# Kernel optimization log

Hardware: AMD Instinct MI355X
Metric: run time of the kernel (lower is better)

Reference implementation:

```python
import jax, jax.numpy as jnp
import numpy as np

MUL = 128                      # multiplicity per irrep
DIMS = (1, 3, 5)               # 2l+1 for l = 0, 1, 2
OFFS = (0, MUL, MUL * 4)       # start offsets of each l-block
TOT = MUL * 9                  # 1152 = total irrep dim
NM = 3 * MUL                   # num_mul = 384


def _split(x):
    # x: [B, 1152] -> list of [B, 128, 2l+1]
    return [x[:, OFFS[i]:OFFS[i] + MUL * DIMS[i]].reshape(-1, MUL, DIMS[i]) for i in range(3)]


def _merge(parts):
    return jnp.concatenate([p.reshape(p.shape[0], -1) for p in parts], axis=-1)


def irrep_linear(x, W, b0):
    # e3nn o3.Linear: per-l mixing of multiplicities, / sqrt(fan_in), bias on scalars only
    parts = _split(x)
    out = [jnp.einsum('nui,uv->nvi', parts[i], W[i]) / np.sqrt(MUL) for i in range(3)]
    out = [out[0] + b0[None, :, None], out[1], out[2]]
    return _merge(out)


def norm_gate_fn(x, W1, b1, W2, b2):
    # QHNet NormGate: [scalars | per-channel norms] -> MLP -> gate non-scalar channels
    parts = _split(x)
    x0 = parts[0][:, :, 0]
    n1 = jnp.sqrt(jnp.sum(parts[1] ** 2, axis=-1))
    n2 = jnp.sqrt(jnp.sum(parts[2] ** 2, axis=-1))
    f0 = jnp.concatenate([x0, n1, n2], axis=-1)          # [B, 384]
    g = jax.nn.silu(f0 @ W1 + b1) @ W2 + b2              # [B, 384]
    g0, g1, g2 = g[:, :MUL], g[:, MUL:2 * MUL], g[:, 2 * MUL:]
    return _merge([g0[:, :, None], parts[1] * g1[:, :, None], parts[2] * g2[:, :, None]])


def ssp(x):
    # shifted softplus
    return jax.nn.softplus(x) - np.log(2.0)


def setup_inputs() -> dict:
    key = jax.random.key(0)
    ks = jax.random.split(key, 24)
    N, E, EA, H = 4096, 65536, 64, 8
    f32 = jnp.float32
    inp = {}
    inp['node_attr'] = jax.random.normal(ks[0], (N, TOT), f32)
    inp['edge_attr'] = jax.random.uniform(ks[1], (E, EA), f32)
    inp['dst'] = jax.random.randint(ks[2], (E,), 0, N)
    inp['src'] = jax.random.randint(ks[3], (E,), 0, N)
    inp['node_pair_attr'] = jax.random.normal(ks[4], (E, TOT), f32)
    # irrep linears (linear_node_pair_inner, linear_node_pair_n, linear_node_pair)
    inp['W_inner'] = jax.random.normal(ks[5], (3, MUL, MUL), f32)
    inp['b_inner'] = jnp.zeros((MUL,), f32)
    inp['W_n'] = jax.random.normal(ks[6], (3, MUL, MUL), f32)
    inp['b_n'] = jnp.zeros((MUL,), f32)
    inp['W_out'] = jax.random.normal(ks[7], (3, MUL, MUL), f32)
    inp['b_out'] = jnp.zeros((MUL,), f32)
    # norm_gate_pre MLP
    inp['ng_pre_W1'] = jax.random.normal(ks[8], (NM, NM), f32) / np.sqrt(NM)
    inp['ng_pre_b1'] = jnp.zeros((NM,), f32)
    inp['ng_pre_W2'] = jax.random.normal(ks[9], (NM, NM), f32) / np.sqrt(NM)
    inp['ng_pre_b2'] = jnp.zeros((NM,), f32)
    # norm_gate MLP
    inp['ng_W1'] = jax.random.normal(ks[10], (NM, NM), f32) / np.sqrt(NM)
    inp['ng_b1'] = jnp.zeros((NM,), f32)
    inp['ng_W2'] = jax.random.normal(ks[11], (NM, NM), f32) / np.sqrt(NM)
    inp['ng_b2'] = jnp.zeros((NM,), f32)
    # fc_node_pair: e3nn FullyConnectedNet [64, 8, 128], no biases, /sqrt(fan_in) in fwd
    inp['fcE_W1'] = jax.random.normal(ks[12], (EA, H), f32)
    inp['fcE_W2'] = jax.random.normal(ks[13], (H, MUL), f32)
    # self.fc: Linear(384,128) + SiLU + Linear(128,128)
    inp['fc_W1'] = jax.random.normal(ks[14], (NM, MUL), f32) / np.sqrt(NM)
    inp['fc_b1'] = jnp.zeros((MUL,), f32)
    inp['fc_W2'] = jax.random.normal(ks[15], (MUL, MUL), f32) / np.sqrt(MUL)
    inp['fc_b2'] = jnp.zeros((MUL,), f32)
    return inp


def reference(node_attr, edge_attr, dst, src, node_pair_attr,
              W_inner, b_inner, W_n, b_n, W_out, b_out,
              ng_pre_W1, ng_pre_b1, ng_pre_W2, ng_pre_b2,
              ng_W1, ng_b1, ng_W2, ng_b2,
              fcE_W1, fcE_W2, fc_W1, fc_b1, fc_W2, fc_b2):
    # s0: scalar invariants from inner products of gathered pair features
    na0 = irrep_linear(node_attr, W_inner, b_inner)
    p_d, p_s = _split(na0[dst]), _split(na0[src])
    ip1 = jnp.sum(p_d[1] * p_s[1], axis=-1) / np.sqrt(3.0)   # [E, 128]
    ip2 = jnp.sum(p_d[2] * p_s[2], axis=-1) / np.sqrt(5.0)   # [E, 128]
    s0 = jnp.concatenate([0.5 * (p_d[0][:, :, 0] + p_s[0][:, :, 0]), ip1, ip2], axis=-1)  # [E, 384]

    na = norm_gate_fn(node_attr, ng_pre_W1, ng_pre_b1, ng_pre_W2, ng_pre_b2)
    na = irrep_linear(na, W_n, b_n)

    # edge gate: e3nn FCN (ssp, /sqrt(fan_in), no bias) * torch MLP(SiLU)
    we = ssp(edge_attr @ fcE_W1 / np.sqrt(edge_attr.shape[-1])) @ fcE_W2 / np.sqrt(fcE_W1.shape[-1])
    ws = jax.nn.silu(s0 @ fc_W1 + fc_b1) @ fc_W2 + fc_b2
    w = we * ws                                              # [E, 128]
    E = w.shape[0]
    total_orb = TOT // MUL                                   # 9
    w_full = jnp.broadcast_to(w[:, :, None], (E, MUL, total_orb)).reshape(E, TOT)

    node_pair = (na[src] + na[dst]) * w_full
    node_pair = norm_gate_fn(node_pair, ng_W1, ng_b1, ng_W2, ng_b2)
    node_pair = irrep_linear(node_pair, W_out, b_out)
    return node_pair + node_pair_attr                        # resnet
```

## Files before the change

### kernel.cpp

```cpp
#include <hip/hip_runtime.h>
#include <cmath>


typedef unsigned short u16;
typedef __bf16 v8bf __attribute__((ext_vector_type(8)));
typedef float  v4f  __attribute__((ext_vector_type(4)));

#define NN 4096
#define EE 65536

__device__ __forceinline__ float b2f(u16 u) {
    union { float f; unsigned i; } x; x.i = ((unsigned)u) << 16; return x.f;
}
__device__ __forceinline__ u16 f2b(float f) {
    union { float f; unsigned i; } x; x.f = f;
    unsigned i = x.i;
    return (u16)((i + 0x7FFFu + ((i >> 16) & 1u)) >> 16);
}

struct GemmP {
    const u16* A; int lda;
    const u16* Bt;
    int M, K, N;
    float alpha;
    const float* bias;
    u16* outB;
    const u16* mult;
    const float* add;
    float* outF;
};

template <int EPI>
__global__ __launch_bounds__(256)
void gemm_k(GemmP p) {
    __shared__ __attribute__((aligned(16))) u16 Al[64][40];
    __shared__ __attribute__((aligned(16))) u16 Bl[64][40];

    const int m0 = blockIdx.x * 64;
    const int n0 = blockIdx.y * 64;
    const int t  = threadIdx.x;
    const int lane = t & 63;
    const int wid  = t >> 6;
    const int wm = (wid & 1) * 32;
    const int wn = (wid >> 1) * 32;
    const int sm = t >> 2;
    const int sk = (t & 3) * 8;
    const int fr = lane & 15;
    const int q  = lane >> 4;

    v4f acc[2][2] = {};

    const u16* Ag = p.A  + (size_t)(m0 + sm) * p.lda + sk;
    const u16* Bg = p.Bt + (size_t)(n0 + sm) * p.K   + sk;

    for (int k0 = 0; k0 < p.K; k0 += 32) {
        uint4 av = *(const uint4*)(Ag + k0);
        uint4 bv = *(const uint4*)(Bg + k0);
        __syncthreads();
        *(uint4*)(&Al[sm][sk]) = av;
        *(uint4*)(&Bl[sm][sk]) = bv;
        __syncthreads();
        v8bf a0 = *(const v8bf*)(&Al[wm +      fr][q * 8]);
        v8bf a1 = *(const v8bf*)(&Al[wm + 16 + fr][q * 8]);
        v8bf b0 = *(const v8bf*)(&Bl[wn +      fr][q * 8]);
        v8bf b1 = *(const v8bf*)(&Bl[wn + 16 + fr][q * 8]);
        acc[0][0] = __builtin_amdgcn_mfma_f32_16x16x32_bf16(a0, b0, acc[0][0], 0, 0, 0);
        acc[0][1] = __builtin_amdgcn_mfma_f32_16x16x32_bf16(a0, b1, acc[0][1], 0, 0, 0);
        acc[1][0] = __builtin_amdgcn_mfma_f32_16x16x32_bf16(a1, b0, acc[1][0], 0, 0, 0);
        acc[1][1] = __builtin_amdgcn_mfma_f32_16x16x32_bf16(a1, b1, acc[1][1], 0, 0, 0);
    }

#pragma unroll
    for (int i = 0; i < 2; i++) {
#pragma unroll
        for (int j = 0; j < 2; j++) {
            const int colg = n0 + wn + j * 16 + fr;
            const float bc = p.bias ? p.bias[colg] : 0.0f;
#pragma unroll
            for (int r = 0; r < 4; r++) {
                const int rowg = m0 + wm + i * 16 + q * 4 + r;
                float v = acc[i][j][r] * p.alpha + bc;
                if constexpr (EPI == 0) {
                    p.outB[(size_t)rowg * p.N + colg] = f2b(v);
                } else if constexpr (EPI == 1) {
                    v = v / (1.0f + __expf(-v));
                    p.outB[(size_t)rowg * p.N + colg] = f2b(v);
                } else if constexpr (EPI == 2) {
                    v *= b2f(p.mult[(size_t)rowg * p.N + colg]);
                    p.outB[(size_t)rowg * p.N + colg] = f2b(v);
                } else {
                    constexpr int DIM = (EPI == 3) ? 1 : ((EPI == 4) ? 3 : 5);
                    constexpr int OFF = (EPI == 3) ? 0 : ((EPI == 4) ? 128 : 512);
                    const int e  = rowg / DIM;
                    const int ii = rowg - e * DIM;
                    const size_t idx = (size_t)e * 1152 + OFF + colg * DIM + ii;
                    p.outF[idx] = v + p.add[idx];
                }
            }
        }
    }
}

struct CvtP { const float* src[15]; u16* dst[15]; int K[15]; int N[15]; };

__global__ void cvt_k(CvtP p) {
    const int j = blockIdx.y;
    const float* s = p.src[j];
    u16* d = p.dst[j];
    const int K = p.K[j], N = p.N[j], tot = K * N;
    for (int idx = blockIdx.x * blockDim.x + threadIdx.x; idx < tot;
         idx += gridDim.x * blockDim.x) {
        const int n = idx / K, k = idx - n * K;
        d[idx] = f2b(s[(size_t)k * N + n]);
    }
}

__global__ void node_prep_k(const float* __restrict__ na, u16* __restrict__ x1p,
                            u16* __restrict__ x2p, u16* __restrict__ f0n) {
    const int idx = blockIdx.x * blockDim.x + threadIdx.x;
    if (idx >= NN * 128) return;
    const int n = idx >> 7, u = idx & 127;
    const float* row = na + (size_t)n * 1152;
    f0n[(size_t)n * 384 + u] = f2b(row[u]);
    float s1 = 0.f;
#pragma unroll
    for (int i = 0; i < 3; i++) {
        float v = row[128 + u * 3 + i];
        x1p[((size_t)(n * 3 + i)) * 128 + u] = f2b(v);
        s1 += v * v;
    }
    f0n[(size_t)n * 384 + 128 + u] = f2b(sqrtf(s1));
    float s2 = 0.f;
#pragma unroll
    for (int i = 0; i < 5; i++) {
        float v = row[512 + u * 5 + i];
        x2p[((size_t)(n * 5 + i)) * 128 + u] = f2b(v);
        s2 += v * v;
    }
    f0n[(size_t)n * 384 + 256 + u] = f2b(sqrtf(s2));
}

__global__ void node_gate_k(const float* __restrict__ na, const u16* __restrict__ gn,
                            u16* __restrict__ h1p, u16* __restrict__ h2p) {
    const int idx = blockIdx.x * blockDim.x + threadIdx.x;
    if (idx >= NN * 128) return;
    const int n = idx >> 7, u = idx & 127;
    const float* row = na + (size_t)n * 1152;
    const float g1 = b2f(gn[(size_t)n * 384 + 128 + u]);
#pragma unroll
    for (int i = 0; i < 3; i++)
        h1p[((size_t)(n * 3 + i)) * 128 + u] = f2b(row[128 + u * 3 + i] * g1);
    const float g2 = b2f(gn[(size_t)n * 384 + 256 + u]);
#pragma unroll
    for (int i = 0; i < 5; i++)
        h2p[((size_t)(n * 5 + i)) * 128 + u] = f2b(row[512 + u * 5 + i] * g2);
}

__global__ void we_k(const float* __restrict__ ea, const float* __restrict__ W1,
                     const float* __restrict__ W2, u16* __restrict__ we) {
    const int lane = threadIdx.x & 63;
    const int e = blockIdx.x * 4 + (threadIdx.x >> 6);
    const float a = ea[(size_t)e * 64 + lane];
    float t8[8];
#pragma unroll
    for (int h = 0; h < 8; h++) {
        float s = a * W1[lane * 8 + h];
#pragma unroll
        for (int m = 1; m < 64; m <<= 1) s += __shfl_xor(s, m, 64);
        const float x = s * 0.125f;
        const float sp = (x > 20.f) ? x : log1pf(__expf(x));
        t8[h] = sp - 0.6931471805599453f;
    }
    float v0 = 0.f, v1 = 0.f;
#pragma unroll
    for (int h = 0; h < 8; h++) {
        v0 += t8[h] * W2[h * 128 + lane];
        v1 += t8[h] * W2[h * 128 + 64 + lane];
    }
    we[(size_t)e * 128 + lane]      = f2b(v0 * 0.3535533905932738f);
    we[(size_t)e * 128 + 64 + lane] = f2b(v1 * 0.3535533905932738f);
}

__global__ void s0_k(const int* __restrict__ dst, const int* __restrict__ src,
                     const u16* __restrict__ na0_0, const u16* __restrict__ na0_1p,
                     const u16* __restrict__ na0_2p, u16* __restrict__ s0) {
    const int e = blockIdx.x, u = threadIdx.x;
    const int d = dst[e], s = src[e];
    const float v0 = 0.5f * (b2f(na0_0[(size_t)d * 128 + u]) + b2f(na0_0[(size_t)s * 128 + u]));
    float ip1 = 0.f;
#pragma unroll
    for (int i = 0; i < 3; i++)
        ip1 += b2f(na0_1p[((size_t)(d * 3 + i)) * 128 + u]) *
               b2f(na0_1p[((size_t)(s * 3 + i)) * 128 + u]);
    float ip2 = 0.f;
#pragma unroll
    for (int i = 0; i < 5; i++)
        ip2 += b2f(na0_2p[((size_t)(d * 5 + i)) * 128 + u]) *
               b2f(na0_2p[((size_t)(s * 5 + i)) * 128 + u]);
    s0[(size_t)e * 384 + u]       = f2b(v0);
    s0[(size_t)e * 384 + 128 + u] = f2b(ip1 * 0.57735026918962576f);
    s0[(size_t)e * 384 + 256 + u] = f2b(ip2 * 0.44721359549995794f);
}

__global__ void pair_k(const int* __restrict__ dst, const int* __restrict__ src,
                       const u16* __restrict__ na_0, const u16* __restrict__ na_1p,
                       const u16* __restrict__ na_2p, const u16* __restrict__ w,
                       u16* __restrict__ f0e, u16* __restrict__ np1p,
                       u16* __restrict__ np2p) {
    __shared__ float wr[128];
    const int e = blockIdx.x, u = threadIdx.x;
    wr[u] = b2f(w[(size_t)e * 128 + u]);
    __syncthreads();
    const int d = dst[e], s = src[e];
    const float v0 = (b2f(na_0[(size_t)d * 128 + u]) + b2f(na_0[(size_t)s * 128 + u])) * wr[u / 9];
    f0e[(size_t)e * 384 + u] = f2b(v0);
    float n1 = 0.f;
#pragma unroll
    for (int i = 0; i < 3; i++) {
        const int t = 128 + u * 3 + i;
        const float v = (b2f(na_1p[((size_t)(d * 3 + i)) * 128 + u]) +
                         b2f(na_1p[((size_t)(s * 3 + i)) * 128 + u])) * wr[t / 9];
        np1p[((size_t)(e * 3 + i)) * 128 + u] = f2b(v);
        n1 += v * v;
    }
    f0e[(size_t)e * 384 + 128 + u] = f2b(sqrtf(n1));
    float n2 = 0.f;
#pragma unroll
    for (int i = 0; i < 5; i++) {
        const int t = 512 + u * 5 + i;
        const float v = (b2f(na_2p[((size_t)(d * 5 + i)) * 128 + u]) +
                         b2f(na_2p[((size_t)(s * 5 + i)) * 128 + u])) * wr[t / 9];
        np2p[((size_t)(e * 5 + i)) * 128 + u] = f2b(v);
        n2 += v * v;
    }
    f0e[(size_t)e * 384 + 256 + u] = f2b(sqrtf(n2));
}

__global__ void gate_k(const u16* __restrict__ ge, u16* __restrict__ np1p,
                       u16* __restrict__ np2p) {
    const int idx = blockIdx.x * blockDim.x + threadIdx.x;
    if (idx >= EE * 128) return;
    const int e = idx >> 7, u = idx & 127;
    const float g1 = b2f(ge[(size_t)e * 384 + 128 + u]);
#pragma unroll
    for (int i = 0; i < 3; i++) {
        const size_t pth = ((size_t)(e * 3 + i)) * 128 + u;
        np1p[pth] = f2b(b2f(np1p[pth]) * g1);
    }
    const float g2 = b2f(ge[(size_t)e * 384 + 256 + u]);
#pragma unroll
    for (int i = 0; i < 5; i++) {
        const size_t pth = ((size_t)(e * 5 + i)) * 128 + u;
        np2p[pth] = f2b(b2f(np2p[pth]) * g2);
    }
}

static inline void launch_gemm(hipStream_t st, int epi, const u16* A, int lda,
                               const u16* Bt, int M, int K, int N, float alpha,
                               const float* bias, u16* outB, const u16* mult,
                               const float* add, float* outF) {
    GemmP p{A, lda, Bt, M, K, N, alpha, bias, outB, mult, add, outF};
    dim3 g(M / 64, N / 64), b(256);
    switch (epi) {
        case 0: gemm_k<0><<<g, b, 0, st>>>(p); break;
        case 1: gemm_k<1><<<g, b, 0, st>>>(p); break;
        case 2: gemm_k<2><<<g, b, 0, st>>>(p); break;
        case 3: gemm_k<3><<<g, b, 0, st>>>(p); break;
        case 4: gemm_k<4><<<g, b, 0, st>>>(p); break;
        case 5: gemm_k<5><<<g, b, 0, st>>>(p); break;
    }
}

extern "C" void kernel_launch(void* const* d_in, const int* in_sizes, int n_in,
                              void* d_out, int out_size, void* d_ws, size_t ws_size,
                              hipStream_t stream) {
    (void)in_sizes; (void)n_in; (void)out_size; (void)ws_size;
    const float* node_attr = (const float*)d_in[0];
    const float* edge_attr = (const float*)d_in[1];
    const int*   dst       = (const int*)d_in[2];
    const int*   src       = (const int*)d_in[3];
    const float* npa       = (const float*)d_in[4];
    const float* W_inner   = (const float*)d_in[5];
    const float* b_inner   = (const float*)d_in[6];
    const float* W_n       = (const float*)d_in[7];
    const float* b_n       = (const float*)d_in[8];
    const float* W_out     = (const float*)d_in[9];
    const float* b_out     = (const float*)d_in[10];
    const float* pre_W1    = (const float*)d_in[11];
    const float* pre_b1    = (const float*)d_in[12];
    const float* pre_W2    = (const float*)d_in[13];
    const float* pre_b2    = (const float*)d_in[14];
    const float* ng_W1     = (const float*)d_in[15];
    const float* ng_b1     = (const float*)d_in[16];
    const float* ng_W2     = (const float*)d_in[17];
    const float* ng_b2     = (const float*)d_in[18];
    const float* fcE_W1    = (const float*)d_in[19];
    const float* fcE_W2    = (const float*)d_in[20];
    const float* fc_W1     = (const float*)d_in[21];
    const float* fc_b1     = (const float*)d_in[22];
    const float* fc_W2     = (const float*)d_in[23];
    const float* fc_b2     = (const float*)d_in[24];
    float* out = (float*)d_out;
    u16* W = (u16*)d_ws;

    u16* wbT_inner = W;
    u16* wbT_n     = W + 49152;
    u16* wbT_out   = W + 98304;
    u16* wbT_pre1  = W + 147456;
    u16* wbT_pre2  = W + 294912;
    u16* wbT_ng1   = W + 442368;
    u16* wbT_ng2   = W + 589824;
    u16* wbT_fc1   = W + 737280;
    u16* wbT_fc2   = W + 786432;
    u16* R1   = W + 802816;
    u16* x1p  = R1;
    u16* x2p  = R1 + 1572864;
    u16* f0n  = R1 + 4194304;
    u16* t1n  = R1 + 5767168;
    u16* gn   = R1 + 7340032;
    u16* hn1p = R1 + 8912896;
    u16* hn2p = R1 + 10485760;
    u16* s0   = R1;
    u16* t1e  = R1;
    u16* na0_0  = W + 25968640;
    u16* na0_1p = na0_0 + 524288;
    u16* na0_2p = na0_1p + 1572864;
    u16* na_0   = na0_2p + 2621440;
    u16* na_1p  = na_0 + 524288;
    u16* na_2p  = na_1p + 1572864;
    u16* ws1    = na_2p + 2621440;
    u16* weB    = ws1 + 8388608;
    u16* wB     = weB + 8388608;
    u16* f0e    = wB + 8388608;
    u16* ge     = f0e;
    u16* np1p   = f0e + 25165824;
    u16* np2p   = np1p + 25165824;

    const float ISQ = 0.08838834764831845f;

    CvtP cp;
    const float* srcs[15] = {W_inner, W_inner + 16384, W_inner + 32768,
                             W_n, W_n + 16384, W_n + 32768,
                             W_out, W_out + 16384, W_out + 32768,
                             pre_W1, pre_W2, ng_W1, ng_W2, fc_W1, fc_W2};
    u16* dsts[15] = {wbT_inner, wbT_inner + 16384, wbT_inner + 32768,
                     wbT_n, wbT_n + 16384, wbT_n + 32768,
                     wbT_out, wbT_out + 16384, wbT_out + 32768,
                     wbT_pre1, wbT_pre2, wbT_ng1, wbT_ng2, wbT_fc1, wbT_fc2};
    const int Ks[15] = {128,128,128,128,128,128,128,128,128,384,384,384,384,384,128};
    const int Ns[15] = {128,128,128,128,128,128,128,128,128,384,384,384,384,128,128};
    for (int j = 0; j < 15; j++) { cp.src[j]=srcs[j]; cp.dst[j]=dsts[j]; cp.K[j]=Ks[j]; cp.N[j]=Ns[j]; }
    cvt_k<<<dim3(64, 15), dim3(256), 0, stream>>>(cp);

    node_prep_k<<<dim3(2048), dim3(256), 0, stream>>>(node_attr, x1p, x2p, f0n);

    launch_gemm(stream, 0, f0n, 384, wbT_inner,          4096, 128, 128, ISQ, b_inner, na0_0, 0, 0, 0);
    launch_gemm(stream, 0, x1p, 128, wbT_inner + 16384, 12288, 128, 128, ISQ, nullptr, na0_1p, 0, 0, 0);
    launch_gemm(stream, 0, x2p, 128, wbT_inner + 32768, 20480, 128, 128, ISQ, nullptr, na0_2p, 0, 0, 0);

    launch_gemm(stream, 1, f0n, 384, wbT_pre1, 4096, 384, 384, 1.f, pre_b1, t1n, 0, 0, 0);
    launch_gemm(stream, 0, t1n, 384, wbT_pre2, 4096, 384, 384, 1.f, pre_b2, gn, 0, 0, 0);
    node_gate_k<<<dim3(2048), dim3(256), 0, stream>>>(node_attr, gn, hn1p, hn2p);

    launch_gemm(stream, 0, gn,   384, wbT_n,          4096, 128, 128, ISQ, b_n,     na_0,  0, 0, 0);
    launch_gemm(stream, 0, hn1p, 128, wbT_n + 16384, 12288, 128, 128, ISQ, nullptr, na_1p, 0, 0, 0);
    launch_gemm(stream, 0, hn2p, 128, wbT_n + 32768, 20480, 128, 128, ISQ, nullptr, na_2p, 0, 0, 0);

    we_k<<<dim3(EE / 4), dim3(256), 0, stream>>>(edge_attr, fcE_W1, fcE_W2, weB);

    s0_k<<<dim3(EE), dim3(128), 0, stream>>>(dst, src, na0_0, na0_1p, na0_2p, s0);

    launch_gemm(stream, 1, s0,  384, wbT_fc1, EE, 384, 128, 1.f, fc_b1, ws1, 0,   0, 0);
    launch_gemm(stream, 2, ws1, 128, wbT_fc2, EE, 128, 128, 1.f, fc_b2, wB,  weB, 0, 0);

    pair_k<<<dim3(EE), dim3(128), 0, stream>>>(dst, src, na_0, na_1p, na_2p, wB, f0e, np1p, np2p);

    launch_gemm(stream, 1, f0e, 384, wbT_ng1, EE, 384, 384, 1.f, ng_b1, t1e, 0, 0, 0);
    launch_gemm(stream, 0, t1e, 384, wbT_ng2, EE, 384, 384, 1.f, ng_b2, ge,  0, 0, 0);
    gate_k<<<dim3(32768), dim3(256), 0, stream>>>(ge, np1p, np2p);

    launch_gemm(stream, 3, ge,   384, wbT_out,          EE,     128, 128, ISQ, b_out,   0, 0, npa, out);
    launch_gemm(stream, 4, np1p, 128, wbT_out + 16384,  EE * 3, 128, 128, ISQ, nullptr, 0, 0, npa, out);
    launch_gemm(stream, 5, np2p, 128, wbT_out + 32768,  EE * 5, 128, 128, ISQ, nullptr, 0, 0, npa, out);
}
```

Baseline: 1.225 ms.

## Fuse edge pair gather, norm-gate MLP, gating and output linear into one kernel

Result: no change. 1.221 ms (-0.3%).

```diff
diff --git a/kernel.cpp b/kernel.cpp
--- a/kernel.cpp
+++ b/kernel.cpp
@@ -8,6 +8,8 @@
 
 #define NN 4096
 #define EE 65536
+
+#define MFMA16 __builtin_amdgcn_mfma_f32_16x16x32_bf16
 
 __device__ __forceinline__ float b2f(u16 u) {
     union { float f; unsigned i; } x; x.i = ((unsigned)u) << 16; return x.f;
@@ -26,8 +28,6 @@
     const float* bias;
     u16* outB;
     const u16* mult;
-    const float* add;
-    float* outF;
 };
 
 template <int EPI>
@@ -64,10 +64,10 @@
         v8bf a1 = *(const v8bf*)(&Al[wm + 16 + fr][q * 8]);
         v8bf b0 = *(const v8bf*)(&Bl[wn +      fr][q * 8]);
         v8bf b1 = *(const v8bf*)(&Bl[wn + 16 + fr][q * 8]);
-        acc[0][0] = __builtin_amdgcn_mfma_f32_16x16x32_bf16(a0, b0, acc[0][0], 0, 0, 0);
-        acc[0][1] = __builtin_amdgcn_mfma_f32_16x16x32_bf16(a0, b1, acc[0][1], 0, 0, 0);
-        acc[1][0] = __builtin_amdgcn_mfma_f32_16x16x32_bf16(a1, b0, acc[1][0], 0, 0, 0);
-        acc[1][1] = __builtin_amdgcn_mfma_f32_16x16x32_bf16(a1, b1, acc[1][1], 0, 0, 0);
+        acc[0][0] = MFMA16(a0, b0, acc[0][0], 0, 0, 0);
+        acc[0][1] = MFMA16(a0, b1, acc[0][1], 0, 0, 0);
+        acc[1][0] = MFMA16(a1, b0, acc[1][0], 0, 0, 0);
+        acc[1][1] = MFMA16(a1, b1, acc[1][1], 0, 0, 0);
     }
 
 #pragma unroll
@@ -85,16 +85,9 @@
                 } else if constexpr (EPI == 1) {
                     v = v / (1.0f + __expf(-v));
                     p.outB[(size_t)rowg * p.N + colg] = f2b(v);
-                } else if constexpr (EPI == 2) {
+                } else {
                     v *= b2f(p.mult[(size_t)rowg * p.N + colg]);
                     p.outB[(size_t)rowg * p.N + colg] = f2b(v);
-                } else {
-                    constexpr int DIM = (EPI == 3) ? 1 : ((EPI == 4) ? 3 : 5);
-                    constexpr int OFF = (EPI == 3) ? 0 : ((EPI == 4) ? 128 : 512);
-                    const int e  = rowg / DIM;
-                    const int ii = rowg - e * DIM;
-                    const size_t idx = (size_t)e * 1152 + OFF + colg * DIM + ii;
-                    p.outF[idx] = v + p.add[idx];
                 }
             }
         }
@@ -202,72 +195,256 @@
     s0[(size_t)e * 384 + 256 + u] = f2b(ip2 * 0.44721359549995794f);
 }
 
-__global__ void pair_k(const int* __restrict__ dst, const int* __restrict__ src,
-                       const u16* __restrict__ na_0, const u16* __restrict__ na_1p,
-                       const u16* __restrict__ na_2p, const u16* __restrict__ w,
-                       u16* __restrict__ f0e, u16* __restrict__ np1p,
-                       u16* __restrict__ np2p) {
-    __shared__ float wr[128];
-    const int e = blockIdx.x, u = threadIdx.x;
-    wr[u] = b2f(w[(size_t)e * 128 + u]);
+__global__ __launch_bounds__(256, 2)
+void edge_fused_k(const int* __restrict__ dst, const int* __restrict__ src,
+                  const u16* __restrict__ na_0, const u16* __restrict__ na_1p,
+                  const u16* __restrict__ na_2p, const u16* __restrict__ wB,
+                  const u16* __restrict__ W1t, const float* __restrict__ b1,
+                  const u16* __restrict__ W2t, const float* __restrict__ b2,
+                  const u16* __restrict__ Wot, const float* __restrict__ bo,
+                  const float* __restrict__ npa, float* __restrict__ out) {
+    __shared__ __attribute__((aligned(16))) u16 bufA[32][392];
+    __shared__ __attribute__((aligned(16))) u16 bufN[21760];
+    __shared__ int dstS[32], srcS[32];
+    __shared__ u16 wS[32][128];
+
+    u16 (*T1)[392]   = (u16 (*)[392])bufN;
+    u16 (*NP)[136]   = (u16 (*)[136])bufN;
+    float (*STG)[68] = (float (*)[68])bufN;
+
+    const int e0 = blockIdx.x * 32;
+    const int t = threadIdx.x;
+    const int lane = t & 63, wid = t >> 6;
+    const int fr = lane & 15, q = lane >> 4;
+    const float ISQ = 0.08838834764831845f;
+
+    if (t < 32) { dstS[t] = dst[e0 + t]; srcS[t] = src[e0 + t]; }
+#pragma unroll
+    for (int rep = 0; rep < 16; rep++) {
+        const int idx = rep * 256 + t;
+        ((u16*)wS)[idx] = wB[(size_t)e0 * 128 + idx];
+    }
     __syncthreads();
-    const int d = dst[e], s = src[e];
-    const float v0 = (b2f(na_0[(size_t)d * 128 + u]) + b2f(na_0[(size_t)s * 128 + u])) * wr[u / 9];
-    f0e[(size_t)e * 384 + u] = f2b(v0);
-    float n1 = 0.f;
-#pragma unroll
-    for (int i = 0; i < 3; i++) {
-        const int t = 128 + u * 3 + i;
+
+    for (int rep = 0; rep < 16; rep++) {
+        const int idx = rep * 256 + t;
+        const int e = idx >> 7, u = idx & 127;
+        const int d = dstS[e], s = srcS[e];
+        const float v0 = (b2f(na_0[(size_t)d * 128 + u]) + b2f(na_0[(size_t)s * 128 + u]))
+                         * b2f(wS[e][u / 9]);
+        bufA[e][u] = f2b(v0);
+        float n1 = 0.f;
+#pragma unroll
+        for (int i = 0; i < 3; i++) {
+            const float v = (b2f(na_1p[((size_t)(d * 3 + i)) * 128 + u]) +
+                             b2f(na_1p[((size_t)(s * 3 + i)) * 128 + u]))
+                            * b2f(wS[e][(128 + u * 3 + i) / 9]);
+            n1 += v * v;
+        }
+        bufA[e][128 + u] = f2b(sqrtf(n1));
+        float n2 = 0.f;
+#pragma unroll
+        for (int i = 0; i < 5; i++) {
+            const float v = (b2f(na_2p[((size_t)(d * 5 + i)) * 128 + u]) +
+                             b2f(na_2p[((size_t)(s * 5 + i)) * 128 + u]))
+                            * b2f(wS[e][(512 + u * 5 + i) / 9]);
+            n2 += v * v;
+        }
+        bufA[e][256 + u] = f2b(sqrtf(n2));
+    }
+    __syncthreads();
+
+    {
+        const int wn = wid * 96;
+        v4f acc[2][6] = {};
+        for (int k0 = 0; k0 < 384; k0 += 32) {
+            const v8bf a0 = *(const v8bf*)&bufA[fr][k0 + q * 8];
+            const v8bf a1 = *(const v8bf*)&bufA[16 + fr][k0 + q * 8];
+#pragma unroll
+            for (int j = 0; j < 6; j++) {
+                const v8bf b = *(const v8bf*)(W1t + (size_t)(wn + j * 16 + fr) * 384 + k0 + q * 8);
+                acc[0][j] = MFMA16(a0, b, acc[0][j], 0, 0, 0);
+                acc[1][j] = MFMA16(a1, b, acc[1][j], 0, 0, 0);
+            }
+        }
+#pragma unroll
+        for (int i = 0; i < 2; i++)
+#pragma unroll
+            for (int j = 0; j < 6; j++) {
+                const int col = wn + j * 16 + fr;
+                const float bb = b1[col];
+#pragma unroll
+                for (int r = 0; r < 4; r++) {
+                    const float v = acc[i][j][r] + bb;
+                    T1[i * 16 + q * 4 + r][col] = f2b(v / (1.f + __expf(-v)));
+                }
+            }
+    }
+    __syncthreads();
+
+    {
+        const int wn = wid * 96;
+        v4f acc[2][6] = {};
+        for (int k0 = 0; k0 < 384; k0 += 32) {
+            const v8bf a0 = *(const v8bf*)&T1[fr][k0 + q * 8];
+            const v8bf a1 = *(const v8bf*)&T1[16 + fr][k0 + q * 8];
+#pragma unroll
+            for (int j = 0; j < 6; j++) {
+                const v8bf b = *(const v8bf*)(W2t + (size_t)(wn + j * 16 + fr) * 384 + k0 + q * 8);
+                acc[0][j] = MFMA16(a0, b, acc[0][j], 0, 0, 0);
+                acc[1][j] = MFMA16(a1, b, acc[1][j], 0, 0, 0);
+            }
+        }
+#pragma unroll
+        for (int i = 0; i < 2; i++)
+#pragma unroll
+            for (int j = 0; j < 6; j++) {
+                const int col = wn + j * 16 + fr;
+                const float bb = b2[col];
+#pragma unroll
+                for (int r = 0; r < 4; r++)
+                    bufA[i * 16 + q * 4 + r][col] = f2b(acc[i][j][r] + bb);
+            }
+    }
+    __syncthreads();
+
+    {
+        const int wn = wid * 32;
+        v4f acc[2][2] = {};
+        for (int k0 = 0; k0 < 128; k0 += 32) {
+            const v8bf a0 = *(const v8bf*)&bufA[fr][k0 + q * 8];
+            const v8bf a1 = *(const v8bf*)&bufA[16 + fr][k0 + q * 8];
+#pragma unroll
+            for (int j = 0; j < 2; j++) {
+                const v8bf b = *(const v8bf*)(Wot + (size_t)(wn + j * 16 + fr) * 128 + k0 + q * 8);
+                acc[0][j] = MFMA16(a0, b, acc[0][j], 0, 0, 0);
+                acc[1][j] = MFMA16(a1, b, acc[1][j], 0, 0, 0);
+            }
+        }
+#pragma unroll
+        for (int i = 0; i < 2; i++)
+#pragma unroll
+            for (int j = 0; j < 2; j++) {
+                const int col = wn + j * 16 + fr;
+                const float bb = bo[col];
+#pragma unroll
+                for (int r = 0; r < 4; r++) {
+                    const size_t o = (size_t)(e0 + i * 16 + q * 4 + r) * 1152 + col;
+                    out[o] = acc[i][j][r] * ISQ + bb + npa[o];
+                }
+            }
+    }
+
+    for (int rep = 0; rep < 48; rep++) {
+        const int idx = rep * 256 + t;
+        const int row = idx >> 7, u = idx & 127;
+        const int e = row / 3, i = row - e * 3;
+        const int d = dstS[e], s = srcS[e];
         const float v = (b2f(na_1p[((size_t)(d * 3 + i)) * 128 + u]) +
-                         b2f(na_1p[((size_t)(s * 3 + i)) * 128 + u])) * wr[t / 9];
-        np1p[((size_t)(e * 3 + i)) * 128 + u] = f2b(v);
-        n1 += v * v;
-    }
-    f0e[(size_t)e * 384 + 128 + u] = f2b(sqrtf(n1));
-    float n2 = 0.f;
-#pragma unroll
-    for (int i = 0; i < 5; i++) {
-        const int t = 512 + u * 5 + i;
+                         b2f(na_1p[((size_t)(s * 3 + i)) * 128 + u]))
+                        * b2f(wS[e][(128 + u * 3 + i) / 9]);
+        NP[row][u] = f2b(v * b2f(bufA[e][128 + u]));
+    }
+    __syncthreads();
+    {
+        const int wm = (wid & 1) * 48, wn = (wid >> 1) * 64;
+        const u16* Wo1 = Wot + 16384;
+        v4f acc[3][4] = {};
+        for (int k0 = 0; k0 < 128; k0 += 32) {
+            v8bf a[3];
+#pragma unroll
+            for (int mi = 0; mi < 3; mi++)
+                a[mi] = *(const v8bf*)&NP[wm + mi * 16 + fr][k0 + q * 8];
+#pragma unroll
+            for (int j = 0; j < 4; j++) {
+                const v8bf b = *(const v8bf*)(Wo1 + (size_t)(wn + j * 16 + fr) * 128 + k0 + q * 8);
+#pragma unroll
+                for (int mi = 0; mi < 3; mi++) acc[mi][j] = MFMA16(a[mi], b, acc[mi][j], 0, 0, 0);
+            }
+        }
+        __syncthreads();
+        for (int h = 0; h < 2; h++) {
+            if ((wid >> 1) == h) {
+#pragma unroll
+                for (int mi = 0; mi < 3; mi++)
+#pragma unroll
+                    for (int j = 0; j < 4; j++)
+#pragma unroll
+                        for (int r = 0; r < 4; r++)
+                            STG[wm + mi * 16 + q * 4 + r][j * 16 + fr] = acc[mi][j][r] * ISQ;
+            }
+            __syncthreads();
+            for (int rep = 0; rep < 24; rep++) {
+                const int idx = rep * 256 + t;
+                const int e = idx / 192, p = idx - e * 192;
+                const int c = p / 3, i = p - c * 3;
+                const size_t o = (size_t)(e0 + e) * 1152 + 128 + h * 192 + p;
+                out[o] = STG[e * 3 + i][c] + npa[o];
+            }
+            __syncthreads();
+        }
+    }
+
+    for (int rep = 0; rep < 80; rep++) {
+        const int idx = rep * 256 + t;
+        const int row = idx >> 7, u = idx & 127;
+        const int e = row / 5, i = row - e * 5;
+        const int d = dstS[e], s = srcS[e];
         const float v = (b2f(na_2p[((size_t)(d * 5 + i)) * 128 + u]) +
-                         b2f(na_2p[((size_t)(s * 5 + i)) * 128 + u])) * wr[t / 9];
-        np2p[((size_t)(e * 5 + i)) * 128 + u] = f2b(v);
-        n2 += v * v;
-    }
-    f0e[(size_t)e * 384 + 256 + u] = f2b(sqrtf(n2));
-}
-
-__global__ void gate_k(const u16* __restrict__ ge, u16* __restrict__ np1p,
-                       u16* __restrict__ np2p) {
-    const int idx = blockIdx.x * blockDim.x + threadIdx.x;
-    if (idx >= EE * 128) return;
-    const int e = idx >> 7, u = idx & 127;
-    const float g1 = b2f(ge[(size_t)e * 384 + 128 + u]);
-#pragma unroll
-    for (int i = 0; i < 3; i++) {
-        const size_t pth = ((size_t)(e * 3 + i)) * 128 + u;
-        np1p[pth] = f2b(b2f(np1p[pth]) * g1);
-    }
-    const float g2 = b2f(ge[(size_t)e * 384 + 256 + u]);
-#pragma unroll
-    for (int i = 0; i < 5; i++) {
-        const size_t pth = ((size_t)(e * 5 + i)) * 128 + u;
-        np2p[pth] = f2b(b2f(np2p[pth]) * g2);
+                         b2f(na_2p[((size_t)(s * 5 + i)) * 128 + u]))
+                        * b2f(wS[e][(512 + u * 5 + i) / 9]);
+        NP[row][u] = f2b(v * b2f(bufA[e][256 + u]));
+    }
+    __syncthreads();
+    {
+        const int wm = (wid & 1) * 80, wn = (wid >> 1) * 64;
+        const u16* Wo2 = Wot + 32768;
+        v4f acc[5][4] = {};
+        for (int k0 = 0; k0 < 128; k0 += 32) {
+            v8bf a[5];
+#pragma unroll
+            for (int mi = 0; mi < 5; mi++)
+                a[mi] = *(const v8bf*)&NP[wm + mi * 16 + fr][k0 + q * 8];
+#pragma unroll
+            for (int j = 0; j < 4; j++) {
+                const v8bf b = *(const v8bf*)(Wo2 + (size_t)(wn + j * 16 + fr) * 128 + k0 + q * 8);
+#pragma unroll
+                for (int mi = 0; mi < 5; mi++) acc[mi][j] = MFMA16(a[mi], b, acc[mi][j], 0, 0, 0);
+            }
+        }
+        __syncthreads();
+        for (int h = 0; h < 2; h++) {
+            if ((wid >> 1) == h) {
+#pragma unroll
+                for (int mi = 0; mi < 5; mi++)
+#pragma unroll
+                    for (int j = 0; j < 4; j++)
+#pragma unroll
+                        for (int r = 0; r < 4; r++)
+                            STG[wm + mi * 16 + q * 4 + r][j * 16 + fr] = acc[mi][j][r] * ISQ;
+            }
+            __syncthreads();
+            for (int rep = 0; rep < 40; rep++) {
+                const int idx = rep * 256 + t;
+                const int e = idx / 320, p = idx - e * 320;
+                const int c = p / 5, i = p - c * 5;
+                const size_t o = (size_t)(e0 + e) * 1152 + 512 + h * 320 + p;
+                out[o] = STG[e * 5 + i][c] + npa[o];
+            }
+            __syncthreads();
+        }
     }
 }
 
 static inline void launch_gemm(hipStream_t st, int epi, const u16* A, int lda,
                                const u16* Bt, int M, int K, int N, float alpha,
-                               const float* bias, u16* outB, const u16* mult,
-                               const float* add, float* outF) {
-    GemmP p{A, lda, Bt, M, K, N, alpha, bias, outB, mult, add, outF};
+                               const float* bias, u16* outB, const u16* mult) {
+    GemmP p{A, lda, Bt, M, K, N, alpha, bias, outB, mult};
     dim3 g(M / 64, N / 64), b(256);
     switch (epi) {
         case 0: gemm_k<0><<<g, b, 0, st>>>(p); break;
         case 1: gemm_k<1><<<g, b, 0, st>>>(p); break;
         case 2: gemm_k<2><<<g, b, 0, st>>>(p); break;
-        case 3: gemm_k<3><<<g, b, 0, st>>>(p); break;
-        case 4: gemm_k<4><<<g, b, 0, st>>>(p); break;
-        case 5: gemm_k<5><<<g, b, 0, st>>>(p); break;
     }
 }
 
@@ -321,7 +498,6 @@
     u16* hn1p = R1 + 8912896;
     u16* hn2p = R1 + 10485760;
     u16* s0   = R1;
-    u16* t1e  = R1;
     u16* na0_0  = W + 25968640;
     u16* na0_1p = na0_0 + 524288;
     u16* na0_2p = na0_1p + 1572864;
@@ -331,10 +507,6 @@
     u16* ws1    = na_2p + 2621440;
     u16* weB    = ws1 + 8388608;
     u16* wB     = weB + 8388608;
-    u16* f0e    = wB + 8388608;
-    u16* ge     = f0e;
-    u16* np1p   = f0e + 25165824;
-    u16* np2p   = np1p + 25165824;
 
     const float ISQ = 0.08838834764831845f;
 
@@ -354,32 +526,26 @@
 
     node_prep_k<<<dim3(2048), dim3(256), 0, stream>>>(node_attr, x1p, x2p, f0n);
 
-    launch_gemm(stream, 0, f0n, 384, wbT_inner,          4096, 128, 128, ISQ, b_inner, na0_0, 0, 0, 0);
-    launch_gemm(stream, 0, x1p, 128, wbT_inner + 16384, 12288, 128, 128, ISQ, nullptr, na0_1p, 0, 0, 0);
-    launch_gemm(stream, 0, x2p, 128, wbT_inner + 32768, 20480, 128, 128, ISQ, nullptr, na0_2p, 0, 0, 0);
-
-    launch_gemm(stream, 1, f0n, 384, wbT_pre1, 4096, 384, 384, 1.f, pre_b1, t1n, 0, 0, 0);
-    launch_gemm(stream, 0, t1n, 384, wbT_pre2, 4096, 384, 384, 1.f, pre_b2, gn, 0, 0, 0);
+    launch_gemm(stream, 0, f0n, 384, wbT_inner,          4096, 128, 128, ISQ, b_inner, na0_0, 0);
+    launch_gemm(stream, 0, x1p, 128, wbT_inner + 16384, 12288, 128, 128, ISQ, nullptr, na0_1p, 0);
+    launch_gemm(stream, 0, x2p, 128, wbT_inner + 32768, 20480, 128, 128, ISQ, nullptr, na0_2p, 0);
+
+    launch_gemm(stream, 1, f0n, 384, wbT_pre1, 4096, 384, 384, 1.f, pre_b1, t1n, 0);
+    launch_gemm(stream, 0, t1n, 384, wbT_pre2, 4096, 384, 384, 1.f, pre_b2, gn, 0);
     node_gate_k<<<dim3(2048), dim3(256), 0, stream>>>(node_attr, gn, hn1p, hn2p);
 
-    launch_gemm(stream, 0, gn,   384, wbT_n,          4096, 128, 128, ISQ, b_n,     na_0,  0, 0, 0);
-    launch_gemm(stream, 0, hn1p, 128, wbT_n + 16384, 12288, 128, 128, ISQ, nullptr, na_1p, 0, 0, 0);
-    launch_gemm(stream, 0, hn2p, 128, wbT_n + 32768, 20480, 128, 128, ISQ, nullptr, na_2p, 0, 0, 0);
+    launch_gemm(stream, 0, gn,   384, wbT_n,          4096, 128, 128, ISQ, b_n,     na_0,  0);
+    launch_gemm(stream, 0, hn1p, 128, wbT_n + 16384, 12288, 128, 128, ISQ, nullptr, na_1p, 0);
+    launch_gemm(stream, 0, hn2p, 128, wbT_n + 32768, 20480, 128, 128, ISQ, nullptr, na_2p, 0);
 
     we_k<<<dim3(EE / 4), dim3(256), 0, stream>>>(edge_attr, fcE_W1, fcE_W2, weB);
 
     s0_k<<<dim3(EE), dim3(128), 0, stream>>>(dst, src, na0_0, na0_1p, na0_2p, s0);
 
-    launch_gemm(stream, 1, s0,  384, wbT_fc1, EE, 384, 128, 1.f, fc_b1, ws1, 0,   0, 0);
-    launch_gemm(stream, 2, ws1, 128, wbT_fc2, EE, 128, 128, 1.f, fc_b2, wB,  weB, 0, 0);
-
-    pair_k<<<dim3(EE), dim3(128), 0, stream>>>(dst, src, na_0, na_1p, na_2p, wB, f0e, np1p, np2p);
-
-    launch_gemm(stream, 1, f0e, 384, wbT_ng1, EE, 384, 384, 1.f, ng_b1, t1e, 0, 0, 0);
-    launch_gemm(stream, 0, t1e, 384, wbT_ng2, EE, 384, 384, 1.f, ng_b2, ge,  0, 0, 0);
-    gate_k<<<dim3(32768), dim3(256), 0, stream>>>(ge, np1p, np2p);
-
-    launch_gemm(stream, 3, ge,   384, wbT_out,          EE,     128, 128, ISQ, b_out,   0, 0, npa, out);
-    launch_gemm(stream, 4, np1p, 128, wbT_out + 16384,  EE * 3, 128, 128, ISQ, nullptr, 0, 0, npa, out);
-    launch_gemm(stream, 5, np2p, 128, wbT_out + 32768,  EE * 5, 128, 128, ISQ, nullptr, 0, 0, npa, out);
-}
+    launch_gemm(stream, 1, s0,  384, wbT_fc1, EE, 384, 128, 1.f, fc_b1, ws1, 0);
+    launch_gemm(stream, 2, ws1, 128, wbT_fc2, EE, 128, 128, 1.f, fc_b2, wB,  weB);
+
+    edge_fused_k<<<dim3(EE / 32), dim3(256), 0, stream>>>(
+        dst, src, na_0, na_1p, na_2p, wB,
+        wbT_ng1, ng_b1, wbT_ng2, ng_b2, wbT_out, b_out, npa, out);
+}
```
